# Kernel optimization log

Measured on AMD Instinct MI355X. Metric: run time of the kernel, lower is better.

## Reference

```python
import jax, jax.numpy as jnp
import numpy as np

NUM_USER = 200000
NUM_ITEM = 100000
DIM_E = 64
N_LAYERS = 3
N_INTER = 1000000  # raw sampled interactions (deduped below)
BATCH = 8192
EDGE_DROP = 0.5    # torch uses np.random.random()*1.0; fixed here for determinism
TGT_DROP = 0.5     # self.dropout


def _xavier_uniform(key, shape):
    fan_in, fan_out = shape[0], shape[1]
    b = np.sqrt(6.0 / (fan_in + fan_out)).astype(np.float32)
    return jax.random.uniform(key, shape, jnp.float32, -b, b)


def setup_inputs() -> dict:
    rng = np.random.default_rng(0)
    u = rng.integers(0, NUM_USER, N_INTER).astype(np.int64)
    it = rng.integers(0, NUM_ITEM, N_INTER).astype(np.int64)
    pair = np.unique(u * NUM_ITEM + it)  # dedupe like the dok_matrix update
    u, it = pair // NUM_ITEM, pair % NUM_ITEM
    # symmetric bipartite adjacency A over N = U + I nodes
    rows = np.concatenate([u, it + NUM_USER])
    cols = np.concatenate([it + NUM_USER, u])
    n_nodes = NUM_USER + NUM_ITEM
    deg = np.bincount(rows, minlength=n_nodes).astype(np.float32) + 1e-7
    dinv = np.power(deg, -0.5)
    vals = (dinv[rows] * dinv[cols]).astype(np.float32)  # D^-1/2 A D^-1/2

    key = jax.random.key(0)
    k1, k2, k3, k4 = jax.random.split(key, 4)
    return {
        "user_emb": _xavier_uniform(k1, (NUM_USER, DIM_E)),
        "item_emb": _xavier_uniform(k2, (NUM_ITEM, DIM_E)),
        "adj_vals": jnp.asarray(vals),
        "adj_rows": jnp.asarray(rows),
        "adj_cols": jnp.asarray(cols),
        "users": jax.random.randint(k3, (BATCH,), 0, NUM_USER),
        "items": jax.random.randint(k4, (BATCH,), 0, NUM_ITEM),
    }


def _spmm(rows, cols, vals, x, n_nodes):
    # out[r] = sum_e vals[e] * x[cols[e]] for rows[e] == r  (COO SpMM)
    return jax.ops.segment_sum(vals[:, None] * x[cols], rows, num_segments=n_nodes)


def reference(user_emb, item_emb, adj_vals, adj_rows, adj_cols, users, items):
    n_nodes = user_emb.shape[0] + item_emb.shape[0]
    kd = jax.random.key(1234)
    ke, ku, ki = jax.random.split(kd, 3)

    # sparse edge dropout: floor(1-rate + U[0,1)) keep mask, rescale by 1/(1-rate)
    keep = jnp.floor(1.0 - EDGE_DROP + jax.random.uniform(ke, adj_vals.shape))
    vals = adj_vals * keep * (1.0 / (1.0 - EDGE_DROP))

    x = jnp.concatenate([user_emb, item_emb], axis=0)  # [N, D]
    acc = x
    for _ in range(N_LAYERS):
        x = _spmm(adj_rows, adj_cols, vals, x, n_nodes)
        acc = acc + x
    all_emb = acc / (N_LAYERS + 1)  # mean over the stacked hops

    u_all = all_emb[:user_emb.shape[0]]
    i_all = all_emb[user_emb.shape[0]:]
    u_online = u_all[users]
    i_online = i_all[items]

    # targets: detached copies with standard dropout
    u_t = jax.lax.stop_gradient(u_online)
    i_t = jax.lax.stop_gradient(i_online)
    um = jax.random.bernoulli(ku, 1.0 - TGT_DROP, u_t.shape)
    im = jax.random.bernoulli(ki, 1.0 - TGT_DROP, i_t.shape)
    u_target = jnp.where(um, u_t / (1.0 - TGT_DROP), 0.0)
    i_target = jnp.where(im, i_t / (1.0 - TGT_DROP), 0.0)
    return (u_online, u_target, i_online, i_target)
```

## Files before the change

### kernel.cpp

```cpp
#include <hip/hip_runtime.h>
#include <stdint.h>

__host__ __device__ inline void tf2x32(uint32_t k0, uint32_t k1,
                                       uint32_t x0, uint32_t x1,
                                       uint32_t& o0, uint32_t& o1) {
  const uint32_t ks2 = k0 ^ k1 ^ 0x1BD11BDAu;
  x0 += k0; x1 += k1;
#define TFR(r) { x0 += x1; x1 = (x1 << (r)) | (x1 >> (32 - (r))); x1 ^= x0; }
  TFR(13) TFR(15) TFR(26) TFR(6)
  x0 += k1;  x1 += ks2 + 1u;
  TFR(17) TFR(29) TFR(16) TFR(24)
  x0 += ks2; x1 += k0 + 2u;
  TFR(13) TFR(15) TFR(26) TFR(6)
  x0 += k0;  x1 += k1 + 3u;
  TFR(17) TFR(29) TFR(16) TFR(24)
  x0 += k1;  x1 += ks2 + 4u;
  TFR(13) TFR(15) TFR(26) TFR(6)
  x0 += ks2; x1 += k0 + 5u;
#undef TFR
  o0 = x0; o1 = x1;
}

__host__ __device__ inline uint32_t bits32(uint32_t k0, uint32_t k1, uint32_t idx) {
  uint32_t a, b;
  tf2x32(k0, k1, 0u, idx, a, b);
  return a ^ b;
}

__device__ inline bool edge_kept(uint32_t k0, uint32_t k1, uint32_t e) {
  return (bits32(k0, k1, e) >> 31) != 0u;
}

__device__ inline float bf_lo(uint32_t u) { return __uint_as_float(u << 16); }
__device__ inline float bf_hi(uint32_t u) { return __uint_as_float(u & 0xffff0000u); }
__device__ inline uint32_t bf_pack(float a, float b) {
  uint32_t lo = (__float_as_uint(a) + 0x8000u) >> 16;
  uint32_t hi = (__float_as_uint(b) + 0x8000u) & 0xffff0000u;
  return hi | lo;
}

__device__ inline void fma8_f32(float a[8], float v, const float4& x0, const float4& x1) {
  a[0] = fmaf(v, x0.x, a[0]); a[1] = fmaf(v, x0.y, a[1]);
  a[2] = fmaf(v, x0.z, a[2]); a[3] = fmaf(v, x0.w, a[3]);
  a[4] = fmaf(v, x1.x, a[4]); a[5] = fmaf(v, x1.y, a[5]);
  a[6] = fmaf(v, x1.z, a[6]); a[7] = fmaf(v, x1.w, a[7]);
}
__device__ inline void fma8_bf(float a[8], float v, const uint4& u) {
  a[0] = fmaf(v, bf_lo(u.x), a[0]); a[1] = fmaf(v, bf_hi(u.x), a[1]);
  a[2] = fmaf(v, bf_lo(u.y), a[2]); a[3] = fmaf(v, bf_hi(u.y), a[3]);
  a[4] = fmaf(v, bf_lo(u.z), a[4]); a[5] = fmaf(v, bf_hi(u.z), a[5]);
  a[6] = fmaf(v, bf_lo(u.w), a[6]); a[7] = fmaf(v, bf_hi(u.w), a[7]);
}

__global__ void k_count(const int* __restrict__ rows, int nnz, int* __restrict__ cnt,
                        uint32_t ke0, uint32_t ke1) {
  int e = blockIdx.x * 256 + threadIdx.x;
  if (e >= nnz) return;
  if (edge_kept(ke0, ke1, (uint32_t)e)) atomicAdd(&cnt[rows[e]], 1);
}

__global__ void k_blocksum(const int* __restrict__ cnt, int n, int* __restrict__ bsum) {
  __shared__ int s[256];
  int i = blockIdx.x * 256 + threadIdx.x;
  s[threadIdx.x] = (i < n) ? cnt[i] : 0;
  __syncthreads();
  for (int off = 128; off > 0; off >>= 1) {
    if (threadIdx.x < off) s[threadIdx.x] += s[threadIdx.x + off];
    __syncthreads();
  }
  if (threadIdx.x == 0) bsum[blockIdx.x] = s[0];
}

__device__ inline void scan_block_1024(const int* __restrict__ bsum, int nb,
                                       int* __restrict__ bpref,
                                       int* a, int* b) {
  int t = threadIdx.x;
  for (int i = t; i < 2048; i += 1024) a[i] = (i < nb) ? bsum[i] : 0;
  __syncthreads();
  int* cur = a; int* nxt = b;
  for (int off = 1; off < 2048; off <<= 1) {
    for (int i = t; i < 2048; i += 1024)
      nxt[i] = cur[i] + (i >= off ? cur[i - off] : 0);
    __syncthreads();
    int* tmp = cur; cur = nxt; nxt = tmp;
  }
  for (int i = t; i <= nb; i += 1024)
    bpref[i] = (i == 0) ? 0 : cur[i - 1];
  __syncthreads();
}

__global__ void k_scanb(const int* __restrict__ bsum, int nb, int* __restrict__ bpref) {
  __shared__ int a[2048], b[2048];
  scan_block_1024(bsum, nb, bpref, a, b);
}

__global__ void k_scan_write(const int* __restrict__ cnt, int n, const int* __restrict__ bpref,
                             int* __restrict__ row_ptr, int* __restrict__ nextc) {
  __shared__ int a[256], b[256];
  int t = threadIdx.x;
  int i = blockIdx.x * 256 + t;
  int v = (i < n) ? cnt[i] : 0;
  a[t] = v;
  __syncthreads();
  int* cur = a; int* nxt = b;
  for (int off = 1; off < 256; off <<= 1) {
    nxt[t] = cur[t] + (t >= off ? cur[t - off] : 0);
    __syncthreads();
    int* tmp = cur; cur = nxt; nxt = tmp;
  }
  int incl = cur[t] + bpref[blockIdx.x];
  int excl = incl - v;
  if (i < n) { row_ptr[i] = excl; nextc[i] = excl; }
  if (i == n - 1) row_ptr[n] = incl;
}

__global__ void k_scatter(const float* __restrict__ avals, const int* __restrict__ rows,
                          const int* __restrict__ cols, int nnz, int* __restrict__ nextc,
                          int2* __restrict__ slot, uint32_t ke0, uint32_t ke1) {
  int e = blockIdx.x * 256 + threadIdx.x;
  if (e >= nnz) return;
  if (!edge_kept(ke0, ke1, (uint32_t)e)) return;
  int r = rows[e];
  int k = atomicAdd(&nextc[r], 1);
  slot[k] = make_int2(cols[e], __float_as_int(avals[e] * 2.0f));
}

__global__ void k_mark_batch(const int* __restrict__ users, const int* __restrict__ items,
                             int batch, int nu, uint8_t* fB, uint8_t* f1, uint8_t* f2) {
  int i = blockIdx.x * 256 + threadIdx.x;
  if (i >= 2 * batch) return;
  int r = (i < batch) ? users[i] : nu + items[i - batch];
  fB[r] = 1; f1[r] = 1; f2[r] = 1;
}

__global__ void k_mark_neighbors(const uint8_t* __restrict__ fin,
                                 const int* __restrict__ row_ptr,
                                 const int2* __restrict__ slot, int n,
                                 uint8_t* __restrict__ fout) {
  int r = blockIdx.x * 256 + threadIdx.x;
  if (r >= n) return;
  if (!fin[r]) return;
  int s = row_ptr[r], e = row_ptr[r + 1];
  for (int k = s; k < e; ++k) fout[slot[k].x] = 1;
}

__global__ void k_flagsum2(const uint8_t* __restrict__ f1, const uint8_t* __restrict__ f2,
                           int n, int* __restrict__ bsum1, int* __restrict__ bsum2) {
  __shared__ int s1[256], s2[256];
  int i = blockIdx.x * 256 + threadIdx.x;
  s1[threadIdx.x] = (i < n) ? (int)f1[i] : 0;
  s2[threadIdx.x] = (i < n) ? (int)f2[i] : 0;
  __syncthreads();
  for (int off = 128; off > 0; off >>= 1) {
    if (threadIdx.x < off) {
      s1[threadIdx.x] += s1[threadIdx.x + off];
      s2[threadIdx.x] += s2[threadIdx.x + off];
    }
    __syncthreads();
  }
  if (threadIdx.x == 0) { bsum1[blockIdx.x] = s1[0]; bsum2[blockIdx.x] = s2[0]; }
}

__global__ void k_scanb2(const int* __restrict__ bsum1, const int* __restrict__ bsum2,
                         int nb, int* __restrict__ bpref1, int* __restrict__ bpref2) {
  __shared__ int a[2048], b[2048];
  scan_block_1024(bsum1, nb, bpref1, a, b);
  scan_block_1024(bsum2, nb, bpref2, a, b);
}

__global__ void k_compact2(const uint8_t* __restrict__ f1, const uint8_t* __restrict__ f2,
                           int n, const int* __restrict__ bpref1,
                           const int* __restrict__ bpref2,
                           int* __restrict__ list1, int* __restrict__ list2) {
  __shared__ int a[256], b[256];
  int t = threadIdx.x;
  int i = blockIdx.x * 256 + t;

  int v = (i < n) ? (int)f1[i] : 0;
  a[t] = v;
  __syncthreads();
  int* cur = a; int* nxt = b;
  for (int off = 1; off < 256; off <<= 1) {
    nxt[t] = cur[t] + (t >= off ? cur[t - off] : 0);
    __syncthreads();
    int* tmp = cur; cur = nxt; nxt = tmp;
  }
  if (v) list1[bpref1[blockIdx.x] + cur[t] - 1] = i;
  __syncthreads();

  v = (i < n) ? (int)f2[i] : 0;
  a[t] = v;
  __syncthreads();
  cur = a; nxt = b;
  for (int off = 1; off < 256; off <<= 1) {
    nxt[t] = cur[t] + (t >= off ? cur[t - off] : 0);
    __syncthreads();
    int* tmp = cur; cur = nxt; nxt = tmp;
  }
  if (v) list2[bpref2[blockIdx.x] + cur[t] - 1] = i;
}

template <int FIRST>
__global__ __launch_bounds__(256) void k_spmm(
    const int* __restrict__ row_ptr, const int2* __restrict__ slot,
    const uint32_t* __restrict__ xin, const float* __restrict__ uemb,
    const float* __restrict__ iemb, uint32_t* __restrict__ xout,
    const int* __restrict__ rowlist, const int* __restrict__ nrows_p, int nu) {
  int nrows = *nrows_p;
  int i = blockIdx.x * 32 + (threadIdx.x >> 3);
  if (i >= nrows) return;
  int r = rowlist[i];
  int j = threadIdx.x & 7;
  int s = row_ptr[r], e = row_ptr[r + 1];
  float a[8] = {0, 0, 0, 0, 0, 0, 0, 0};
  for (int k = s; k < e; k += 2) {
    int2 s0 = slot[k];
    bool has1 = (k + 1 < e);
    int2 s1 = slot[has1 ? k + 1 : k];
    float v0 = __int_as_float(s0.y);
    float v1 = has1 ? __int_as_float(s1.y) : 0.0f;
    if (FIRST) {
      const float* p0 = (s0.x < nu) ? uemb + (size_t)s0.x * 64
                                    : iemb + (size_t)(s0.x - nu) * 64;
      const float* p1 = (s1.x < nu) ? uemb + (size_t)s1.x * 64
                                    : iemb + (size_t)(s1.x - nu) * 64;
      float4 xa0 = *(const float4*)(p0 + 8 * j);
      float4 xb0 = *(const float4*)(p0 + 8 * j + 4);
      float4 xa1 = *(const float4*)(p1 + 8 * j);
      float4 xb1 = *(const float4*)(p1 + 8 * j + 4);
      fma8_f32(a, v0, xa0, xb0);
      fma8_f32(a, v1, xa1, xb1);
    } else {
      uint4 u0 = *(const uint4*)(xin + (size_t)s0.x * 32 + 4 * j);
      uint4 u1 = *(const uint4*)(xin + (size_t)s1.x * 32 + 4 * j);
      fma8_bf(a, v0, u0);
      fma8_bf(a, v1, u1);
    }
  }
  uint4 o;
  o.x = bf_pack(a[0], a[1]); o.y = bf_pack(a[2], a[3]);
  o.z = bf_pack(a[4], a[5]); o.w = bf_pack(a[6], a[7]);
  *(uint4*)(xout + (size_t)r * 32 + 4 * j) = o;
}

__global__ __launch_bounds__(256) void k_spmm_gather(
    const int* __restrict__ row_ptr, const int2* __restrict__ slot,
    const uint32_t* __restrict__ xin, const int* __restrict__ users,
    const int* __restrict__ items, float* __restrict__ out,
    int batch, int nu) {
  int b = blockIdx.x * 32 + (threadIdx.x >> 3);
  if (b >= 2 * batch) return;
  int j = threadIdx.x & 7;
  size_t H = (size_t)batch * 64;
  int r; size_t dst;
  if (b < batch) {
    r = users[b];
    dst = (size_t)b * 64;
  } else {
    int bi = b - batch;
    r = nu + items[bi];
    dst = 2 * H + (size_t)bi * 64;
  }
  int s = row_ptr[r], e = row_ptr[r + 1];
  float a[8] = {0, 0, 0, 0, 0, 0, 0, 0};
  for (int k = s; k < e; k += 2) {
    int2 s0 = slot[k];
    bool has1 = (k + 1 < e);
    int2 s1 = slot[has1 ? k + 1 : k];
    float v0 = __int_as_float(s0.y);
    float v1 = has1 ? __int_as_float(s1.y) : 0.0f;
    uint4 u0 = *(const uint4*)(xin + (size_t)s0.x * 32 + 4 * j);
    uint4 u1 = *(const uint4*)(xin + (size_t)s1.x * 32 + 4 * j);
    fma8_bf(a, v0, u0);
    fma8_bf(a, v1, u1);
  }
  float* o = out + dst + 8 * j;
  float4 t0 = *(float4*)o;
  float4 t1 = *(float4*)(o + 4);
  t0.x += a[0]; t0.y += a[1]; t0.z += a[2]; t0.w += a[3];
  t1.x += a[4]; t1.y += a[5]; t1.z += a[6]; t1.w += a[7];
  *(float4*)o = t0;
  *(float4*)(o + 4) = t1;
}

template <int INIT>
__global__ void k_gather(const uint32_t* __restrict__ x, const float* __restrict__ uemb,
                         const float* __restrict__ iemb, const int* __restrict__ users,
                         const int* __restrict__ items, float* __restrict__ out,
                         int batch, int nu) {
  int b = blockIdx.x * 32 + (threadIdx.x >> 3);
  if (b >= 2 * batch) return;
  int j = threadIdx.x & 7;
  size_t H = (size_t)batch * 64;
  int row; size_t dst; bool isu = b < batch;
  if (isu) {
    row = users[b];
    dst = (size_t)b * 64 + 8 * j;
  } else {
    int bi = b - batch;
    row = items[bi];
    dst = 2 * H + (size_t)bi * 64 + 8 * j;
  }
  if (INIT) {
    const float* p = (isu ? uemb + (size_t)row * 64 : iemb + (size_t)row * 64) + 8 * j;
    *(float4*)(out + dst) = *(const float4*)p;
    *(float4*)(out + dst + 4) = *(const float4*)(p + 4);
  } else {
    int xr = isu ? row : nu + row;
    uint4 u = *(const uint4*)(x + (size_t)xr * 32 + 4 * j);
    float* o = out + dst;
    float4 t0 = *(float4*)o;
    float4 t1 = *(float4*)(o + 4);
    t0.x += bf_lo(u.x); t0.y += bf_hi(u.x); t0.z += bf_lo(u.y); t0.w += bf_hi(u.y);
    t1.x += bf_lo(u.z); t1.y += bf_hi(u.z); t1.z += bf_lo(u.w); t1.w += bf_hi(u.w);
    *(float4*)o = t0;
    *(float4*)(o + 4) = t1;
  }
}

__global__ void k_finalize(float* __restrict__ out, int batch,
                           uint32_t ku0, uint32_t ku1, uint32_t ki0, uint32_t ki1) {
  int j = blockIdx.x * 256 + threadIdx.x;
  int H = batch * 64;
  if (j >= 2 * H) return;
  bool is_u = j < H;
  int f = is_u ? j : j - H;
  size_t online = is_u ? (size_t)f : (size_t)2 * H + f;
  uint32_t k0 = is_u ? ku0 : ki0;
  uint32_t k1 = is_u ? ku1 : ki1;
  float o = out[online] * 0.25f;
  bool present = (bits32(k0, k1, (uint32_t)f) >> 31) == 0u;
  out[online] = o;
  out[online + H] = present ? o * 2.0f : 0.0f;
}

extern "C" void kernel_launch(void* const* d_in, const int* in_sizes, int n_in,
                              void* d_out, int out_size, void* d_ws, size_t ws_size,
                              hipStream_t stream) {
  const float* uemb  = (const float*)d_in[0];
  const float* iemb  = (const float*)d_in[1];
  const float* avals = (const float*)d_in[2];
  const int*   rows  = (const int*)d_in[3];
  const int*   cols  = (const int*)d_in[4];
  const int*   users = (const int*)d_in[5];
  const int*   items = (const int*)d_in[6];
  const int DIM = 64;
  const int NU = in_sizes[0] / DIM;
  const int NI = in_sizes[1] / DIM;
  const int NNZ = in_sizes[2];
  const int B = in_sizes[5];
  const int NN = NU + NI;
  float* out = (float*)d_out;
  (void)n_in; (void)out_size; (void)ws_size;

  uint32_t ke0, ke1, ku0, ku1, ki0, ki1;
  tf2x32(0u, 1234u, 0u, 0u, ke0, ke1);
  tf2x32(0u, 1234u, 0u, 1u, ku0, ku1);
  tf2x32(0u, 1234u, 0u, 2u, ki0, ki1);

  char* p = (char*)d_ws;
  auto carve = [&](size_t bytes) {
    char* r = p;
    p += (bytes + 255) & ~(size_t)255;
    return (void*)r;
  };
  uint32_t* X0    = (uint32_t*)carve((size_t)NN * 32 * 4);
  uint32_t* X1    = (uint32_t*)carve((size_t)NN * 32 * 4);
  int2*  slot     = (int2*)carve((size_t)NNZ * 8);
  int*   cnt      = (int*)carve((size_t)NN * 4);
  int*   row_ptr  = (int*)carve((size_t)(NN + 1) * 4);
  int*   nextc    = (int*)carve((size_t)NN * 4);
  uint8_t* fB     = (uint8_t*)carve((size_t)NN * 3);
  uint8_t* f1     = fB + NN;
  uint8_t* f2     = fB + 2 * (size_t)NN;
  int*   list1    = (int*)carve((size_t)NN * 4);
  int*   list2    = (int*)carve((size_t)NN * 4);
  const int NB    = (NN + 255) / 256;
  int*   bsum     = (int*)carve((size_t)NB * 4);
  int*   bpref    = (int*)carve((size_t)(NB + 1) * 4);
  int*   bsum1    = (int*)carve((size_t)NB * 4);
  int*   bpref1   = (int*)carve((size_t)(NB + 1) * 4);
  int*   bsum2    = (int*)carve((size_t)NB * 4);
  int*   bpref2   = (int*)carve((size_t)(NB + 1) * 4);

  hipMemsetAsync(cnt, 0, (size_t)NN * 4, stream);
  hipMemsetAsync(fB, 0, (size_t)NN * 3, stream);

  const int gE = (NNZ + 255) / 256;
  const int gN = (NN + 255) / 256;
  k_count<<<gE, 256, 0, stream>>>(rows, NNZ, cnt, ke0, ke1);
  k_blocksum<<<NB, 256, 0, stream>>>(cnt, NN, bsum);
  k_scanb<<<1, 1024, 0, stream>>>(bsum, NB, bpref);
  k_scan_write<<<NB, 256, 0, stream>>>(cnt, NN, bpref, row_ptr, nextc);
  k_scatter<<<gE, 256, 0, stream>>>(avals, rows, cols, NNZ, nextc, slot, ke0, ke1);

  const int gB = (2 * B + 255) / 256;
  k_mark_batch<<<gB, 256, 0, stream>>>(users, items, B, NU, fB, f1, f2);
  k_mark_neighbors<<<gN, 256, 0, stream>>>(fB, row_ptr, slot, NN, f2);
  k_mark_neighbors<<<gN, 256, 0, stream>>>(f2, row_ptr, slot, NN, f1);
  k_flagsum2<<<NB, 256, 0, stream>>>(f1, f2, NN, bsum1, bsum2);
  k_scanb2<<<1, 1024, 0, stream>>>(bsum1, bsum2, NB, bpref1, bpref2);
  k_compact2<<<NB, 256, 0, stream>>>(f1, f2, NN, bpref1, bpref2, list1, list2);

  const int gG = (2 * B + 31) / 32;
  const int gS = (NN + 31) / 32;

  k_gather<1><<<gG, 256, 0, stream>>>(X0, uemb, iemb, users, items, out, B, NU);

  k_spmm<1><<<gS, 256, 0, stream>>>(row_ptr, slot, X1, uemb, iemb, X0, list1, bpref1 + NB, NU);
  k_gather<0><<<gG, 256, 0, stream>>>(X0, uemb, iemb, users, items, out, B, NU);
  k_spmm<0><<<gS, 256, 0, stream>>>(row_ptr, slot, X0, uemb, iemb, X1, list2, bpref2 + NB, NU);
  k_gather<0><<<gG, 256, 0, stream>>>(X1, uemb, iemb, users, items, out, B, NU);
  k_spmm_gather<<<gG, 256, 0, stream>>>(row_ptr, slot, X1, users, items, out, B, NU);

  const int gF = (2 * B * DIM + 255) / 256;
  k_finalize<<<gF, 256, 0, stream>>>(out, B, ku0, ku1, ki0, ki1);
}
```

Measured before the change: 189.5 us.

## Exploit sorted user-half edges to build user CSR by stream compaction

Splits the adjacency into a user half (rows already sorted, first E/2 edges) and an item half. The user half's CSR is now built with a ballot-based keep bitmask plus a block scan and ordered compaction, so those edges need no atomics. Only the item half still uses atomic counting and scatter. This relies on the input layout where the first half of the edges are user rows in sorted order, and all SpMM and neighbor-marking kernels now branch between the two CSR structures.

```diff
diff --git a/kernel.cpp b/kernel.cpp
--- a/kernel.cpp
+++ b/kernel.cpp
@@ -52,23 +52,29 @@
   a[6] = fmaf(v, bf_lo(u.w), a[6]); a[7] = fmaf(v, bf_hi(u.w), a[7]);
 }
 
-__global__ void k_count(const int* __restrict__ rows, int nnz, int* __restrict__ cnt,
-                        uint32_t ke0, uint32_t ke1) {
-  int e = blockIdx.x * 256 + threadIdx.x;
-  if (e >= nnz) return;
-  if (edge_kept(ke0, ke1, (uint32_t)e)) atomicAdd(&cnt[rows[e]], 1);
-}
-
-__global__ void k_blocksum(const int* __restrict__ cnt, int n, int* __restrict__ bsum) {
-  __shared__ int s[256];
-  int i = blockIdx.x * 256 + threadIdx.x;
-  s[threadIdx.x] = (i < n) ? cnt[i] : 0;
-  __syncthreads();
-  for (int off = 128; off > 0; off >>= 1) {
-    if (threadIdx.x < off) s[threadIdx.x] += s[threadIdx.x + off];
-    __syncthreads();
-  }
-  if (threadIdx.x == 0) bsum[blockIdx.x] = s[0];
+__global__ __launch_bounds__(1024) void k_keep(
+    const int* __restrict__ rows, int E, int E2, int nu,
+    unsigned long long* __restrict__ keepw, int* __restrict__ bsumE,
+    int* __restrict__ cnt, uint32_t ke0, uint32_t ke1) {
+  __shared__ int s[16];
+  int e = blockIdx.x * 1024 + threadIdx.x;
+  int lane = threadIdx.x & 63;
+  int wid = threadIdx.x >> 6;
+  bool kept = (e < E) && edge_kept(ke0, ke1, (uint32_t)e);
+  unsigned long long m = __ballot(kept);
+  int ws = blockIdx.x * 1024 + wid * 64;
+  if (lane == 0 && ws < E) keepw[ws >> 6] = m;
+  int nf = 0;
+  if (ws + 64 <= E2) nf = __popcll(m);
+  else if (ws < E2) nf = __popcll(m & ((1ull << (E2 - ws)) - 1ull));
+  if (lane == 0) s[wid] = nf;
+  __syncthreads();
+  if (threadIdx.x == 0) {
+    int t = 0;
+    for (int i = 0; i < 16; ++i) t += s[i];
+    bsumE[blockIdx.x] = t;
+  }
+  if (kept && e >= E2) atomicAdd(&cnt[rows[e] - nu], 1);
 }
 
 __device__ inline void scan_block_1024(const int* __restrict__ bsum, int nb,
@@ -89,9 +95,23 @@
   __syncthreads();
 }
 
-__global__ void k_scanb(const int* __restrict__ bsum, int nb, int* __restrict__ bpref) {
+__global__ void k_scanb2x(const int* __restrict__ bsumA, int nbA, int* __restrict__ bprefA,
+                          const int* __restrict__ bsumB, int nbB, int* __restrict__ bprefB) {
   __shared__ int a[2048], b[2048];
-  scan_block_1024(bsum, nb, bpref, a, b);
+  scan_block_1024(bsumA, nbA, bprefA, a, b);
+  scan_block_1024(bsumB, nbB, bprefB, a, b);
+}
+
+__global__ void k_blocksum(const int* __restrict__ cnt, int n, int* __restrict__ bsum) {
+  __shared__ int s[256];
+  int i = blockIdx.x * 256 + threadIdx.x;
+  s[threadIdx.x] = (i < n) ? cnt[i] : 0;
+  __syncthreads();
+  for (int off = 128; off > 0; off >>= 1) {
+    if (threadIdx.x < off) s[threadIdx.x] += s[threadIdx.x + off];
+    __syncthreads();
+  }
+  if (threadIdx.x == 0) bsum[blockIdx.x] = s[0];
 }
 
 __global__ void k_scan_write(const int* __restrict__ cnt, int n, const int* __restrict__ bpref,
@@ -114,15 +134,48 @@
   if (i == n - 1) row_ptr[n] = incl;
 }
 
-__global__ void k_scatter(const float* __restrict__ avals, const int* __restrict__ rows,
-                          const int* __restrict__ cols, int nnz, int* __restrict__ nextc,
-                          int2* __restrict__ slot, uint32_t ke0, uint32_t ke1) {
-  int e = blockIdx.x * 256 + threadIdx.x;
-  if (e >= nnz) return;
-  if (!edge_kept(ke0, ke1, (uint32_t)e)) return;
-  int r = rows[e];
+__global__ __launch_bounds__(1024) void k_compactU(
+    const int* __restrict__ rows, const int* __restrict__ cols,
+    const float* __restrict__ avals, const unsigned long long* __restrict__ keepw,
+    const int* __restrict__ bprefE, int E2, int nu, int nbE,
+    int2* __restrict__ uslot, int* __restrict__ row_ptr_u) {
+  __shared__ int a[1024], b[1024];
+  int t = threadIdx.x;
+  int e = blockIdx.x * 1024 + t;
+  bool kept = (e < E2) && ((keepw[e >> 6] >> (e & 63)) & 1ull);
+  a[t] = kept ? 1 : 0;
+  __syncthreads();
+  int* cur = a; int* nxt = b;
+  for (int off = 1; off < 1024; off <<= 1) {
+    nxt[t] = cur[t] + (t >= off ? cur[t - off] : 0);
+    __syncthreads();
+    int* tmp = cur; cur = nxt; nxt = tmp;
+  }
+  int excl = cur[t] - (kept ? 1 : 0);
+  int pos = bprefE[blockIdx.x] + excl;
+  if (kept) uslot[pos] = make_int2(cols[e], __float_as_int(avals[e] * 2.0f));
+  if (e < E2) {
+    int r = rows[e];
+    int rp = (e == 0) ? -1 : rows[e - 1];
+    for (int rr = rp + 1; rr <= r; ++rr) row_ptr_u[rr] = pos;
+    if (e == E2 - 1) {
+      int total = bprefE[nbE];
+      for (int rr = r + 1; rr <= nu; ++rr) row_ptr_u[rr] = total;
+    }
+  }
+}
+
+__global__ void k_scatterI(const int* __restrict__ rows, const int* __restrict__ cols,
+                           const float* __restrict__ avals,
+                           const unsigned long long* __restrict__ keepw,
+                           int E, int E2, int nu, int* __restrict__ nextc,
+                           int2* __restrict__ islot) {
+  int e = E2 + blockIdx.x * 256 + threadIdx.x;
+  if (e >= E) return;
+  if (!((keepw[e >> 6] >> (e & 63)) & 1ull)) return;
+  int r = rows[e] - nu;
   int k = atomicAdd(&nextc[r], 1);
-  slot[k] = make_int2(cols[e], __float_as_int(avals[e] * 2.0f));
+  islot[k] = make_int2(cols[e], __float_as_int(avals[e] * 2.0f));
 }
 
 __global__ void k_mark_batch(const int* __restrict__ users, const int* __restrict__ items,
@@ -134,14 +187,19 @@
 }
 
 __global__ void k_mark_neighbors(const uint8_t* __restrict__ fin,
-                                 const int* __restrict__ row_ptr,
-                                 const int2* __restrict__ slot, int n,
-                                 uint8_t* __restrict__ fout) {
+                                 const int* __restrict__ row_ptr_u,
+                                 const int2* __restrict__ uslot,
+                                 const int* __restrict__ row_ptr_i,
+                                 const int2* __restrict__ islot,
+                                 int n, int nu, uint8_t* __restrict__ fout) {
   int r = blockIdx.x * 256 + threadIdx.x;
   if (r >= n) return;
   if (!fin[r]) return;
-  int s = row_ptr[r], e = row_ptr[r + 1];
-  for (int k = s; k < e; ++k) fout[slot[k].x] = 1;
+  const int* rp = (r < nu) ? row_ptr_u : row_ptr_i;
+  const int2* sl = (r < nu) ? uslot : islot;
+  int rr = (r < nu) ? r : r - nu;
+  int s = rp[rr], e = rp[rr + 1];
+  for (int k = s; k < e; ++k) fout[sl[k].x] = 1;
 }
 
 __global__ void k_flagsum2(const uint8_t* __restrict__ f1, const uint8_t* __restrict__ f2,
@@ -159,13 +217,6 @@
     __syncthreads();
   }
   if (threadIdx.x == 0) { bsum1[blockIdx.x] = s1[0]; bsum2[blockIdx.x] = s2[0]; }
-}
-
-__global__ void k_scanb2(const int* __restrict__ bsum1, const int* __restrict__ bsum2,
-                         int nb, int* __restrict__ bpref1, int* __restrict__ bpref2) {
-  __shared__ int a[2048], b[2048];
-  scan_block_1024(bsum1, nb, bpref1, a, b);
-  scan_block_1024(bsum2, nb, bpref2, a, b);
 }
 
 __global__ void k_compact2(const uint8_t* __restrict__ f1, const uint8_t* __restrict__ f2,
@@ -202,7 +253,8 @@
 
 template <int FIRST>
 __global__ __launch_bounds__(256) void k_spmm(
-    const int* __restrict__ row_ptr, const int2* __restrict__ slot,
+    const int* __restrict__ row_ptr_u, const int2* __restrict__ uslot,
+    const int* __restrict__ row_ptr_i, const int2* __restrict__ islot,
     const uint32_t* __restrict__ xin, const float* __restrict__ uemb,
     const float* __restrict__ iemb, uint32_t* __restrict__ xout,
     const int* __restrict__ rowlist, const int* __restrict__ nrows_p, int nu) {
@@ -211,12 +263,16 @@
   if (i >= nrows) return;
   int r = rowlist[i];
   int j = threadIdx.x & 7;
-  int s = row_ptr[r], e = row_ptr[r + 1];
+  bool isu = r < nu;
+  const int* rp = isu ? row_ptr_u : row_ptr_i;
+  const int2* sl = isu ? uslot : islot;
+  int rr = isu ? r : r - nu;
+  int s = rp[rr], e = rp[rr + 1];
   float a[8] = {0, 0, 0, 0, 0, 0, 0, 0};
   for (int k = s; k < e; k += 2) {
-    int2 s0 = slot[k];
+    int2 s0 = sl[k];
     bool has1 = (k + 1 < e);
-    int2 s1 = slot[has1 ? k + 1 : k];
+    int2 s1 = sl[has1 ? k + 1 : k];
     float v0 = __int_as_float(s0.y);
     float v1 = has1 ? __int_as_float(s1.y) : 0.0f;
     if (FIRST) {
@@ -244,7 +300,8 @@
 }
 
 __global__ __launch_bounds__(256) void k_spmm_gather(
-    const int* __restrict__ row_ptr, const int2* __restrict__ slot,
+    const int* __restrict__ row_ptr_u, const int2* __restrict__ uslot,
+    const int* __restrict__ row_ptr_i, const int2* __restrict__ islot,
     const uint32_t* __restrict__ xin, const int* __restrict__ users,
     const int* __restrict__ items, float* __restrict__ out,
     int batch, int nu) {
@@ -252,21 +309,23 @@
   if (b >= 2 * batch) return;
   int j = threadIdx.x & 7;
   size_t H = (size_t)batch * 64;
-  int r; size_t dst;
+  const int* rp; const int2* sl; int rr; size_t dst;
   if (b < batch) {
-    r = users[b];
+    rr = users[b];
+    rp = row_ptr_u; sl = uslot;
     dst = (size_t)b * 64;
   } else {
     int bi = b - batch;
-    r = nu + items[bi];
+    rr = items[bi];
+    rp = row_ptr_i; sl = islot;
     dst = 2 * H + (size_t)bi * 64;
   }
-  int s = row_ptr[r], e = row_ptr[r + 1];
+  int s = rp[rr], e = rp[rr + 1];
   float a[8] = {0, 0, 0, 0, 0, 0, 0, 0};
   for (int k = s; k < e; k += 2) {
-    int2 s0 = slot[k];
+    int2 s0 = sl[k];
     bool has1 = (k + 1 < e);
-    int2 s1 = slot[has1 ? k + 1 : k];
+    int2 s1 = sl[has1 ? k + 1 : k];
     float v0 = __int_as_float(s0.y);
     float v1 = has1 ? __int_as_float(s1.y) : 0.0f;
     uint4 u0 = *(const uint4*)(xin + (size_t)s0.x * 32 + 4 * j);
@@ -347,7 +406,8 @@
   const int DIM = 64;
   const int NU = in_sizes[0] / DIM;
   const int NI = in_sizes[1] / DIM;
-  const int NNZ = in_sizes[2];
+  const int E  = in_sizes[2];
+  const int E2 = E / 2;
   const int B = in_sizes[5];
   const int NN = NU + NI;
   float* out = (float*)d_out;
@@ -366,40 +426,52 @@
   };
   uint32_t* X0    = (uint32_t*)carve((size_t)NN * 32 * 4);
   uint32_t* X1    = (uint32_t*)carve((size_t)NN * 32 * 4);
-  int2*  slot     = (int2*)carve((size_t)NNZ * 8);
-  int*   cnt      = (int*)carve((size_t)NN * 4);
-  int*   row_ptr  = (int*)carve((size_t)(NN + 1) * 4);
-  int*   nextc    = (int*)carve((size_t)NN * 4);
+  int2*  uslot    = (int2*)carve((size_t)E2 * 8);
+  int2*  islot    = (int2*)carve((size_t)(E - E2) * 8);
+  unsigned long long* keepw = (unsigned long long*)carve(((size_t)E / 64 + 2) * 8);
+  int*   cnt      = (int*)carve((size_t)NI * 4);
+  int*   row_ptr_u = (int*)carve((size_t)(NU + 1) * 4);
+  int*   row_ptr_i = (int*)carve((size_t)(NI + 1) * 4);
+  int*   nextc    = (int*)carve((size_t)NI * 4);
   uint8_t* fB     = (uint8_t*)carve((size_t)NN * 3);
   uint8_t* f1     = fB + NN;
   uint8_t* f2     = fB + 2 * (size_t)NN;
   int*   list1    = (int*)carve((size_t)NN * 4);
   int*   list2    = (int*)carve((size_t)NN * 4);
+  const int GK    = (E + 1023) / 1024;
+  const int NBE   = (E2 + 1023) / 1024;
+  const int NBI   = (NI + 255) / 256;
   const int NB    = (NN + 255) / 256;
-  int*   bsum     = (int*)carve((size_t)NB * 4);
-  int*   bpref    = (int*)carve((size_t)(NB + 1) * 4);
+  int*   bsumE    = (int*)carve((size_t)GK * 4);
+  int*   bprefE   = (int*)carve((size_t)(NBE + 1) * 4);
+  int*   bsumI    = (int*)carve((size_t)NBI * 4);
+  int*   bprefI   = (int*)carve((size_t)(NBI + 1) * 4);
   int*   bsum1    = (int*)carve((size_t)NB * 4);
   int*   bpref1   = (int*)carve((size_t)(NB + 1) * 4);
   int*   bsum2    = (int*)carve((size_t)NB * 4);
   int*   bpref2   = (int*)carve((size_t)(NB + 1) * 4);
 
-  hipMemsetAsync(cnt, 0, (size_t)NN * 4, stream);
+  hipMemsetAsync(cnt, 0, (size_t)NI * 4, stream);
   hipMemsetAsync(fB, 0, (size_t)NN * 3, stream);
 
-  const int gE = (NNZ + 255) / 256;
+  k_keep<<<GK, 1024, 0, stream>>>(rows, E, E2, NU, keepw, bsumE, cnt, ke0, ke1);
+  k_blocksum<<<NBI, 256, 0, stream>>>(cnt, NI, bsumI);
+  k_scanb2x<<<1, 1024, 0, stream>>>(bsumE, NBE, bprefE, bsumI, NBI, bprefI);
+  k_scan_write<<<NBI, 256, 0, stream>>>(cnt, NI, bprefI, row_ptr_i, nextc);
+  k_compactU<<<NBE, 1024, 0, stream>>>(rows, cols, avals, keepw, bprefE, E2, NU, NBE,
+                                       uslot, row_ptr_u);
+  {
+    const int gI = (E - E2 + 255) / 256;
+    k_scatterI<<<gI, 256, 0, stream>>>(rows, cols, avals, keepw, E, E2, NU, nextc, islot);
+  }
+
+  const int gB = (2 * B + 255) / 256;
   const int gN = (NN + 255) / 256;
-  k_count<<<gE, 256, 0, stream>>>(rows, NNZ, cnt, ke0, ke1);
-  k_blocksum<<<NB, 256, 0, stream>>>(cnt, NN, bsum);
-  k_scanb<<<1, 1024, 0, stream>>>(bsum, NB, bpref);
-  k_scan_write<<<NB, 256, 0, stream>>>(cnt, NN, bpref, row_ptr, nextc);
-  k_scatter<<<gE, 256, 0, stream>>>(avals, rows, cols, NNZ, nextc, slot, ke0, ke1);
-
-  const int gB = (2 * B + 255) / 256;
   k_mark_batch<<<gB, 256, 0, stream>>>(users, items, B, NU, fB, f1, f2);
-  k_mark_neighbors<<<gN, 256, 0, stream>>>(fB, row_ptr, slot, NN, f2);
-  k_mark_neighbors<<<gN, 256, 0, stream>>>(f2, row_ptr, slot, NN, f1);
+  k_mark_neighbors<<<gN, 256, 0, stream>>>(fB, row_ptr_u, uslot, row_ptr_i, islot, NN, NU, f2);
+  k_mark_neighbors<<<gN, 256, 0, stream>>>(f2, row_ptr_u, uslot, row_ptr_i, islot, NN, NU, f1);
   k_flagsum2<<<NB, 256, 0, stream>>>(f1, f2, NN, bsum1, bsum2);
-  k_scanb2<<<1, 1024, 0, stream>>>(bsum1, bsum2, NB, bpref1, bpref2);
+  k_scanb2x<<<1, 1024, 0, stream>>>(bsum1, NB, bpref1, bsum2, NB, bpref2);
   k_compact2<<<NB, 256, 0, stream>>>(f1, f2, NN, bpref1, bpref2, list1, list2);
 
   const int gG = (2 * B + 31) / 32;
@@ -407,11 +479,14 @@
 
   k_gather<1><<<gG, 256, 0, stream>>>(X0, uemb, iemb, users, items, out, B, NU);
 
-  k_spmm<1><<<gS, 256, 0, stream>>>(row_ptr, slot, X1, uemb, iemb, X0, list1, bpref1 + NB, NU);
+  k_spmm<1><<<gS, 256, 0, stream>>>(row_ptr_u, uslot, row_ptr_i, islot, X1,
+                                    uemb, iemb, X0, list1, bpref1 + NB, NU);
   k_gather<0><<<gG, 256, 0, stream>>>(X0, uemb, iemb, users, items, out, B, NU);
-  k_spmm<0><<<gS, 256, 0, stream>>>(row_ptr, slot, X0, uemb, iemb, X1, list2, bpref2 + NB, NU);
+  k_spmm<0><<<gS, 256, 0, stream>>>(row_ptr_u, uslot, row_ptr_i, islot, X0,
+                                    uemb, iemb, X1, list2, bpref2 + NB, NU);
   k_gather<0><<<gG, 256, 0, stream>>>(X1, uemb, iemb, users, items, out, B, NU);
-  k_spmm_gather<<<gG, 256, 0, stream>>>(row_ptr, slot, X1, users, items, out, B, NU);
+  k_spmm_gather<<<gG, 256, 0, stream>>>(row_ptr_u, uslot, row_ptr_i, islot, X1,
+                                        users, items, out, B, NU);
 
   const int gF = (2 * B * DIM + 255) / 256;
   k_finalize<<<gF, 256, 0, stream>>>(out, B, ku0, ku1, ki0, ki1);
```

Measured after the change: 175.3 us. 1.08x faster.
